# Optimization experiments

Measured on AMD Instinct MI355X. Metric: run time of the kernel, lower is better.

Reference implementation:

```python
import jax, jax.numpy as jnp
import numpy as np

N_ATOMS = 10000
N_EDGES = 150000
NB = 128          # n_atom_basis
NI = 3            # n_interactions
MAX_Z = 100
N_RBF = 20
CUTOFF = 5.0
EPS = 1e-08
BATCH = 64


def setup_inputs() -> dict:
    key = jax.random.key(0)
    ks = jax.random.split(key, 20)
    f32 = jnp.float32
    s = 0.05
    positions = jax.random.normal(ks[0], (N_ATOMS, 3), f32)
    atomic_numbers = jax.random.randint(ks[1], (N_ATOMS,), 0, MAX_Z)
    idx_i = jax.random.randint(ks[2], (N_EDGES,), 0, N_ATOMS)
    off = jax.random.randint(ks[3], (N_EDGES,), 1, N_ATOMS)
    idx_j = (idx_i + off) % N_ATOMS  # avoid self-edges (d_ij == 0)
    idx_m = jnp.sort(jax.random.randint(ks[4], (N_ATOMS,), 0, BATCH))
    emb = (jax.random.normal(ks[5], (MAX_Z, NB), f32) * s).at[0].set(0.0)  # padding_idx=0
    fW = jax.random.normal(ks[6], (N_RBF, NI * 3 * NB), f32) * s
    fb = jnp.zeros((NI * 3 * NB,), f32)
    ic1_W = jax.random.normal(ks[7], (NI, NB, NB), f32) * s
    ic1_b = jnp.zeros((NI, NB), f32)
    ic2_W = jax.random.normal(ks[8], (NI, NB, 3 * NB), f32) * s
    ic2_b = jnp.zeros((NI, 3 * NB), f32)
    mix_W = jax.random.normal(ks[9], (NI, NB, 2 * NB), f32) * s  # no bias
    ctx1_W = jax.random.normal(ks[10], (NI, 2 * NB, NB), f32) * s
    ctx1_b = jnp.zeros((NI, NB), f32)
    ctx2_W = jax.random.normal(ks[11], (NI, NB, 3 * NB), f32) * s
    ctx2_b = jnp.zeros((NI, 3 * NB), f32)
    o1_W = jax.random.normal(ks[12], (NB, NB), f32) * s
    o1_b = jnp.zeros((NB,), f32)
    o2_W = jax.random.normal(ks[13], (NB, NB), f32) * s
    o2_b = jnp.zeros((NB,), f32)
    o3_W = jax.random.normal(ks[14], (NB, 1), f32) * s
    o3_b = jnp.zeros((1,), f32)
    return dict(positions=positions, emb=emb, fW=fW, fb=fb,
                ic1_W=ic1_W, ic1_b=ic1_b, ic2_W=ic2_W, ic2_b=ic2_b,
                mix_W=mix_W, ctx1_W=ctx1_W, ctx1_b=ctx1_b, ctx2_W=ctx2_W, ctx2_b=ctx2_b,
                o1_W=o1_W, o1_b=o1_b, o2_W=o2_W, o2_b=o2_b, o3_W=o3_W, o3_b=o3_b,
                atomic_numbers=atomic_numbers, idx_i=idx_i, idx_j=idx_j, idx_m=idx_m,
                batch_num=BATCH)


def reference(positions, emb, fW, fb, ic1_W, ic1_b, ic2_W, ic2_b,
              mix_W, ctx1_W, ctx1_b, ctx2_W, ctx2_b,
              o1_W, o1_b, o2_W, o2_b, o3_W, o3_b,
              atomic_numbers, idx_i, idx_j, idx_m, batch_num):
    seg = jax.ops.segment_sum
    n_atoms = positions.shape[0]
    # pairwise distances
    r_ij = positions[idx_j] - positions[idx_i]                      # [E,3]
    d_ij = jnp.sqrt(jnp.sum(r_ij * r_ij, axis=-1, keepdims=True))   # [E,1]
    # Gaussian RBF
    offsets = jnp.linspace(0.0, CUTOFF, N_RBF, dtype=positions.dtype)
    width = offsets[1] - offsets[0]
    coeff = -0.5 / (width * width)
    phi = jnp.exp(coeff * (d_ij[..., None] - offsets) ** 2)         # [E,1,20]
    # cosine cutoff
    fcut = (0.5 * (jnp.cos(d_ij * jnp.pi / CUTOFF) + 1.0) * (d_ij < CUTOFF))[..., None]  # [E,1,1]
    filters = (phi @ fW + fb) * fcut                                # [E,1,NI*3*NB]
    dir_ij = r_ij / d_ij                                            # [E,3]
    q = emb[atomic_numbers][:, None]                                # [N,1,NB]
    mu = jnp.zeros((n_atoms, 3, NB), q.dtype)
    for i in range(NI):
        Wij = filters[..., i * 3 * NB:(i + 1) * 3 * NB]             # [E,1,3*NB]
        # interaction
        x = jax.nn.silu(q @ ic1_W[i] + ic1_b[i]) @ ic2_W[i] + ic2_b[i]  # [N,1,3*NB]
        x = Wij * x[idx_j]                                          # [E,1,3*NB]
        dq, dmuR, dmumu = jnp.split(x, 3, axis=-1)                  # [E,1,NB] each
        dq = seg(dq, idx_i, num_segments=n_atoms)                   # [N,1,NB]
        muj = mu[idx_j]                                             # [E,3,NB]
        dmu = dmuR * dir_ij[:, :, None] + dmumu * muj               # [E,3,NB]
        dmu = seg(dmu, idx_i, num_segments=n_atoms)                 # [N,3,NB]
        q = q + dq
        mu = mu + dmu
        # mixing
        mu_mix = mu @ mix_W[i]                                      # [N,3,2*NB]
        mu_V, mu_Wc = jnp.split(mu_mix, 2, axis=-1)                 # [N,3,NB]
        mu_Vn = jnp.sqrt(jnp.sum(mu_V * mu_V, axis=-2, keepdims=True) + EPS)  # [N,1,NB]
        ctx = jnp.concatenate([q, mu_Vn], axis=-1)                  # [N,1,2*NB]
        x = jax.nn.silu(ctx @ ctx1_W[i] + ctx1_b[i]) @ ctx2_W[i] + ctx2_b[i]  # [N,1,3*NB]
        dq_in, dmu_in, dqmu_in = jnp.split(x, 3, axis=-1)
        dmu_in = dmu_in * mu_Wc                                     # [N,3,NB]
        dqmu_in = dqmu_in * jnp.sum(mu_V * mu_Wc, axis=1, keepdims=True)  # [N,1,NB]
        q = q + dq_in + dqmu_in
        mu = mu + dmu_in
    qf = q[:, 0]                                                    # [N,NB]
    h = jax.nn.silu(qf @ o1_W + o1_b)
    h = jax.nn.silu(h @ o2_W + o2_b)
    y = h @ o3_W + o3_b                                             # [N,1]
    y = seg(y, idx_m, num_segments=batch_num)                       # [B,1]
    return (y, mu)
```

## Files before the change

### kernel.cpp

```cpp
#include <hip/hip_runtime.h>
#include <math.h>

#define NA 10000
#define NE 150000
#define NRBF 20
#define CUT 5.0f
#define EPSV 1e-8f
#define NBATCH 64
#define CAP 48
#define PI_F 3.14159265358979323846f

typedef short bf16x8 __attribute__((ext_vector_type(8)));
typedef float f32x4 __attribute__((ext_vector_type(4)));
typedef __fp16 h16x2 __attribute__((ext_vector_type(2)));
typedef unsigned short u16;

__device__ __forceinline__ u16 f2b(float x) {
    unsigned u = __builtin_bit_cast(unsigned, x);
    return (u16)((u + 0x7FFFu + ((u >> 16) & 1u)) >> 16);
}
__device__ __forceinline__ float b2f(u16 b) {
    unsigned u = ((unsigned)b) << 16;
    return __builtin_bit_cast(float, u);
}
__device__ __forceinline__ float silu_f(float x) { return x / (1.0f + expf(-x)); }

#define P_IC1 0
#define P_IC2 49152
#define P_MIX 196608
#define P_C1  294912
#define P_C2  393216
#define P_O1  540672
#define P_O2  557056
#define P_TOT 573440

__global__ __launch_bounds__(64) void pack_k(
    const float* __restrict__ ic1W, const float* __restrict__ ic2W,
    const float* __restrict__ mixW, const float* __restrict__ c1W,
    const float* __restrict__ c2W, const float* __restrict__ o1W,
    const float* __restrict__ o2W, u16* __restrict__ packs) {
    int id = blockIdx.x;
    const float* src; u16* dst; int N, rel;
    if (id < 96)        { int m = id / 32;          rel = id % 32; src = ic1W + m * 16384; dst = packs + P_IC1 + m * 16384; N = 128; }
    else if (id < 384)  { id -= 96;  int m = id / 96; rel = id % 96; src = ic2W + m * 49152; dst = packs + P_IC2 + m * 49152; N = 384; }
    else if (id < 576)  { id -= 384; int m = id / 64; rel = id % 64; src = mixW + m * 32768; dst = packs + P_MIX + m * 32768; N = 256; }
    else if (id < 768)  { id -= 576; int m = id / 64; rel = id % 64; src = c1W  + m * 32768; dst = packs + P_C1  + m * 32768; N = 128; }
    else if (id < 1056) { id -= 768; int m = id / 96; rel = id % 96; src = c2W  + m * 49152; dst = packs + P_C2  + m * 49152; N = 384; }
    else if (id < 1088) { rel = id - 1056; src = o1W; dst = packs + P_O1; N = 128; }
    else                { rel = id - 1088; src = o2W; dst = packs + P_O2; N = 128; }
    int NBT = N >> 4;
    int kb = rel / NBT, nb = rel % NBT;
    int l = threadIdx.x;
    int col = nb * 16 + (l & 15);
    int k0 = kb * 32 + 8 * (l >> 4);
    u16 v[8];
    #pragma unroll
    for (int i = 0; i < 8; i++) v[i] = f2b(src[(size_t)(k0 + i) * N + col]);
    *(bf16x8*)(dst + rel * 512 + l * 8) = *(bf16x8*)v;
}

template<int MT, int K>
__device__ __forceinline__ void stageA(const float* __restrict__ src, int row0,
                                       int maxrow, u16* As) {
    const int NV = MT * K / 4;
    for (int idx = threadIdx.x; idx < NV; idx += 256) {
        int r = idx / (K / 4), c4 = idx % (K / 4);
        float4 v = make_float4(0.f, 0.f, 0.f, 0.f);
        if (row0 + r < maxrow) v = *(const float4*)(src + (size_t)(row0 + r) * K + c4 * 4);
        uint2 o;
        o.x = (unsigned)f2b(v.x) | ((unsigned)f2b(v.y) << 16);
        o.y = (unsigned)f2b(v.z) | ((unsigned)f2b(v.w) << 16);
        *(uint2*)(As + r * (K + 8) + c4 * 4) = o;
    }
}

__device__ __forceinline__ bf16x8 aFrag(const u16* As, int stride, int row, int k0) {
    return *(const bf16x8*)(As + row * stride + k0);
}
__device__ __forceinline__ bf16x8 bFrag(const u16* __restrict__ pack, int NBT,
                                        int ks, int nb, int l) {
    return *(const bf16x8*)(pack + ((size_t)(ks * NBT + nb) * 64 + l) * 8);
}
#define MFMA(a, b, c) __builtin_amdgcn_mfma_f32_16x16x32_bf16(a, b, c, 0, 0, 0)

__global__ void init_q_k(const float* __restrict__ emb, const int* __restrict__ z,
                         float* __restrict__ q) {
    int idx = blockIdx.x * blockDim.x + threadIdx.x;
    if (idx >= NA * 128) return;
    int a = idx >> 7, c = idx & 127;
    q[idx] = emb[z[a] * 128 + c];
}

__global__ void edge_geom_k(const float* __restrict__ pos,
                            const int* __restrict__ idx_i, const int* __restrict__ idx_j,
                            float* __restrict__ edata, int* __restrict__ cnt,
                            int* __restrict__ bucketj) {
    int e = blockIdx.x * blockDim.x + threadIdx.x;
    if (e >= NE) return;
    int i = idx_i[e], j = idx_j[e];
    float rx = pos[j * 3 + 0] - pos[i * 3 + 0];
    float ry = pos[j * 3 + 1] - pos[i * 3 + 1];
    float rz = pos[j * 3 + 2] - pos[i * 3 + 2];
    float d = sqrtf(rx * rx + ry * ry + rz * rz);
    float inv = 1.0f / d;
    float fc = (d < CUT) ? 0.5f * (cosf(d * PI_F / CUT) + 1.0f) : 0.0f;
    const float width = CUT / (float)(NRBF - 1);
    const float coeff = -0.5f / (width * width);
    float ph[NRBF];
    #pragma unroll
    for (int k = 0; k < NRBF; k++) {
        float t = d - (float)k * width;
        ph[k] = expf(coeff * t * t);
    }
    int slot = atomicAdd(&cnt[i], 1);
    if (slot < CAP) {
        bucketj[i * CAP + slot] = j;
        float* ed = edata + ((size_t)i * CAP + slot) * 16;
        ed[0] = rx * inv; ed[1] = ry * inv; ed[2] = rz * inv; ed[3] = fc;
        h16x2* php = (h16x2*)(ed + 4);
        #pragma unroll
        for (int p = 0; p < 10; p++)
            php[p] = __builtin_amdgcn_cvt_pkrtz(ph[2 * p], ph[2 * p + 1]);
    }
}

__global__ __launch_bounds__(256) void mlp1_k(
    const float* __restrict__ q, const u16* __restrict__ pW1, const float* __restrict__ b1,
    const u16* __restrict__ pW2, const float* __restrict__ b2, u16* __restrict__ x_bf) {
    __shared__ u16 As[32 * 136];
    __shared__ u16 Hs[32 * 136];
    int abase = blockIdx.x * 32;
    stageA<32, 128>(q, abase, NA, As);
    __syncthreads();
    int l = threadIdx.x & 63, w = threadIdx.x >> 6, lm = l & 15, lg = l >> 4;
    f32x4 acc[2][2];
    #pragma unroll
    for (int j = 0; j < 2; j++)
        #pragma unroll
        for (int mi = 0; mi < 2; mi++) acc[j][mi] = (f32x4){0.f, 0.f, 0.f, 0.f};
    #pragma unroll
    for (int ks = 0; ks < 4; ks++) {
        bf16x8 a0 = aFrag(As, 136, lm, ks * 32 + 8 * lg);
        bf16x8 a1 = aFrag(As, 136, 16 + lm, ks * 32 + 8 * lg);
        #pragma unroll
        for (int j = 0; j < 2; j++) {
            bf16x8 b = bFrag(pW1, 8, ks, w + 4 * j, l);
            acc[j][0] = MFMA(a0, b, acc[j][0]);
            acc[j][1] = MFMA(a1, b, acc[j][1]);
        }
    }
    #pragma unroll
    for (int j = 0; j < 2; j++) {
        int col = 16 * (w + 4 * j) + lm;
        float bb = b1[col];
        #pragma unroll
        for (int mi = 0; mi < 2; mi++)
            #pragma unroll
            for (int v = 0; v < 4; v++)
                Hs[(16 * mi + 4 * lg + v) * 136 + col] = f2b(silu_f(acc[j][mi][v] + bb));
    }
    __syncthreads();
    f32x4 acc2[6][2];
    #pragma unroll
    for (int j = 0; j < 6; j++)
        #pragma unroll
        for (int mi = 0; mi < 2; mi++) acc2[j][mi] = (f32x4){0.f, 0.f, 0.f, 0.f};
    #pragma unroll
    for (int ks = 0; ks < 4; ks++) {
        bf16x8 a0 = aFrag(Hs, 136, lm, ks * 32 + 8 * lg);
        bf16x8 a1 = aFrag(Hs, 136, 16 + lm, ks * 32 + 8 * lg);
        #pragma unroll
        for (int j = 0; j < 6; j++) {
            bf16x8 b = bFrag(pW2, 24, ks, w + 4 * j, l);
            acc2[j][0] = MFMA(a0, b, acc2[j][0]);
            acc2[j][1] = MFMA(a1, b, acc2[j][1]);
        }
    }
    #pragma unroll
    for (int j = 0; j < 6; j++) {
        int col = 16 * (w + 4 * j) + lm;
        float bb = b2[col];
        #pragma unroll
        for (int mi = 0; mi < 2; mi++)
            #pragma unroll
            for (int v = 0; v < 4; v++) {
                int ga = abase + 16 * mi + 4 * lg + v;
                if (ga < NA) x_bf[(size_t)ga * 384 + col] = f2b(acc2[j][mi][v] + bb);
            }
    }
}

template<int IT0>
__global__ __launch_bounds__(128) void gather_k(
    const float* __restrict__ fW, const float* __restrict__ fb,
    const u16* __restrict__ x_bf, const u16* __restrict__ mu_bf,
    const float* __restrict__ edata, const int* __restrict__ cnt,
    const int* __restrict__ bucketj, int it,
    float* __restrict__ q, float* __restrict__ muF) {
    int a = blockIdx.x;
    int c = threadIdx.x;
    int cb = it * 384;
    h16x2 wp0[10], wp1[10], wp2[10];
    #pragma unroll
    for (int p = 0; p < 10; p++) {
        const float* r0 = fW + (2 * p) * 1152 + cb;
        const float* r1 = fW + (2 * p + 1) * 1152 + cb;
        wp0[p] = __builtin_amdgcn_cvt_pkrtz(r0[c], r1[c]);
        wp1[p] = __builtin_amdgcn_cvt_pkrtz(r0[128 + c], r1[128 + c]);
        if (!IT0) wp2[p] = __builtin_amdgcn_cvt_pkrtz(r0[256 + c], r1[256 + c]);
    }
    float fb0 = fb[cb + c], fb1 = fb[cb + 128 + c];
    float fb2 = IT0 ? 0.f : fb[cb + 256 + c];
    int n = cnt[a]; if (n > CAP) n = CAP;
    const int* bj = bucketj + a * CAP;
    const float* eb = edata + (size_t)a * CAP * 16;
    float adq = 0.f, am0 = 0.f, am1 = 0.f, am2 = 0.f;
    for (int ei = 0; ei < n; ei++) {
        int j = __builtin_amdgcn_readfirstlane(bj[ei]);
        const float* ed = eb + ei * 16;
        float4 gg = *(const float4*)ed;
        const h16x2* php = (const h16x2*)(ed + 4);
        float f0 = fb0, f1 = fb1, f2 = fb2;
        #pragma unroll
        for (int p = 0; p < 10; p++) {
            h16x2 ph = php[p];
            f0 = __builtin_amdgcn_fdot2(ph, wp0[p], f0, false);
            f1 = __builtin_amdgcn_fdot2(ph, wp1[p], f1, false);
            if (!IT0) f2 = __builtin_amdgcn_fdot2(ph, wp2[p], f2, false);
        }
        f0 *= gg.w; f1 *= gg.w;
        const u16* xr = x_bf + (size_t)j * 384;
        float x0 = f0 * b2f(xr[c]), x1 = f1 * b2f(xr[128 + c]);
        adq += x0;
        am0 += x1 * gg.x;
        am1 += x1 * gg.y;
        am2 += x1 * gg.z;
        if (!IT0) {
            f2 *= gg.w;
            float x2 = f2 * b2f(xr[256 + c]);
            const u16* mr = mu_bf + (size_t)j * 384;
            am0 += x2 * b2f(mr[c]);
            am1 += x2 * b2f(mr[128 + c]);
            am2 += x2 * b2f(mr[256 + c]);
        }
    }
    q[(size_t)a * 128 + c] += adq;
    muF[(size_t)a * 384 + c] += am0;
    muF[(size_t)a * 384 + 128 + c] += am1;
    muF[(size_t)a * 384 + 256 + c] += am2;
}

__global__ __launch_bounds__(256) void mixctx_k(
    float* __restrict__ q, float* __restrict__ muF, u16* __restrict__ mu_bf,
    const u16* __restrict__ pM,
    const u16* __restrict__ pC1, const float* __restrict__ c1b,
    const u16* __restrict__ pC2, const float* __restrict__ c2b) {
    __shared__ u16 As[48 * 136];
    __shared__ u16 mmL[16 * 768];
    __shared__ u16 Cs[16 * 264];
    __shared__ u16 Hs[16 * 136];
    int abase = blockIdx.x * 16;
    stageA<48, 128>(muF, abase * 3, 3 * NA, As);
    __syncthreads();
    int l = threadIdx.x & 63, w = threadIdx.x >> 6, lm = l & 15, lg = l >> 4;
    {
        f32x4 acc[4][3];
        #pragma unroll
        for (int j = 0; j < 4; j++)
            #pragma unroll
            for (int mi = 0; mi < 3; mi++) acc[j][mi] = (f32x4){0.f, 0.f, 0.f, 0.f};
        #pragma unroll
        for (int ks = 0; ks < 4; ks++) {
            bf16x8 a[3];
            #pragma unroll
            for (int mi = 0; mi < 3; mi++) a[mi] = aFrag(As, 136, 16 * mi + lm, ks * 32 + 8 * lg);
            #pragma unroll
            for (int j = 0; j < 4; j++) {
                bf16x8 b = bFrag(pM, 16, ks, w + 4 * j, l);
                #pragma unroll
                for (int mi = 0; mi < 3; mi++) acc[j][mi] = MFMA(a[mi], b, acc[j][mi]);
            }
        }
        #pragma unroll
        for (int j = 0; j < 4; j++) {
            int col = 16 * (w + 4 * j) + lm;
            #pragma unroll
            for (int mi = 0; mi < 3; mi++)
                #pragma unroll
                for (int v = 0; v < 4; v++) {
                    int R = 16 * mi + 4 * lg + v;
                    mmL[(R / 3) * 768 + (R % 3) * 256 + col] = f2b(acc[j][mi][v]);
                }
        }
    }
    __syncthreads();
    for (int idx = threadIdx.x; idx < 16 * 128; idx += 256) {
        int a = idx >> 7, cc = idx & 127;
        int ga = abase + a;
        float s = EPSV;
        #pragma unroll
        for (int d = 0; d < 3; d++) {
            float t = b2f(mmL[a * 768 + d * 256 + cc]);
            s += t * t;
        }
        float qv = (ga < NA) ? q[(size_t)ga * 128 + cc] : 0.f;
        Cs[a * 264 + cc] = f2b(qv);
        Cs[a * 264 + 128 + cc] = f2b(sqrtf(s));
    }
    __syncthreads();
    {
        f32x4 h[2];
        h[0] = (f32x4){0.f, 0.f, 0.f, 0.f}; h[1] = (f32x4){0.f, 0.f, 0.f, 0.f};
        #pragma unroll
        for (int ks = 0; ks < 8; ks++) {
            bf16x8 a0 = aFrag(Cs, 264, lm, ks * 32 + 8 * lg);
            #pragma unroll
            for (int j = 0; j < 2; j++) {
                bf16x8 b = bFrag(pC1, 8, ks, w + 4 * j, l);
                h[j] = MFMA(a0, b, h[j]);
            }
        }
        #pragma unroll
        for (int j = 0; j < 2; j++) {
            int col = 16 * (w + 4 * j) + lm;
            float bb = c1b[col];
            #pragma unroll
            for (int v = 0; v < 4; v++)
                Hs[(4 * lg + v) * 136 + col] = f2b(silu_f(h[j][v] + bb));
        }
    }
    __syncthreads();
    f32x4 acc2[6];
    #pragma unroll
    for (int j = 0; j < 6; j++) acc2[j] = (f32x4){0.f, 0.f, 0.f, 0.f};
    #pragma unroll
    for (int ks = 0; ks < 4; ks++) {
        bf16x8 a0 = aFrag(Hs, 136, lm, ks * 32 + 8 * lg);
        #pragma unroll
        for (int j = 0; j < 6; j++) {
            bf16x8 b = bFrag(pC2, 24, ks, w + 4 * j, l);
            acc2[j] = MFMA(a0, b, acc2[j]);
        }
    }
    #pragma unroll
    for (int j = 0; j < 6; j++) {
        float bb = c2b[16 * (w + 4 * j) + lm];
        #pragma unroll
        for (int v = 0; v < 4; v++) acc2[j][v] += bb;
    }
    #pragma unroll
    for (int v = 0; v < 4; v++) {
        int al = 4 * lg + v;
        int ga = abase + al;
        if (ga >= NA) continue;
        #pragma unroll
        for (int jj = 0; jj < 2; jj++) {
            int cc = 16 * w + 64 * jj + lm;
            float x0 = acc2[jj][v], x1 = acc2[jj + 2][v], x2 = acc2[jj + 4][v];
            float dot = 0.f, muW[3];
            #pragma unroll
            for (int d = 0; d < 3; d++) {
                float muV = b2f(mmL[al * 768 + d * 256 + cc]);
                muW[d] = b2f(mmL[al * 768 + d * 256 + 128 + cc]);
                dot += muV * muW[d];
            }
            q[(size_t)ga * 128 + cc] += x0 + x2 * dot;
            #pragma unroll
            for (int d = 0; d < 3; d++) {
                size_t mo = (size_t)ga * 384 + d * 128 + cc;
                float m = muF[mo] + x1 * muW[d];
                muF[mo] = m;
                mu_bf[mo] = f2b(m);
            }
        }
    }
}

__global__ __launch_bounds__(256) void readout_k(
    const float* __restrict__ q, const u16* __restrict__ pO1, const float* __restrict__ o1b,
    const u16* __restrict__ pO2, const float* __restrict__ o2b,
    const float* __restrict__ o3W, const float* __restrict__ o3b,
    const int* __restrict__ idx_m, float* __restrict__ y) {
    __shared__ u16 As[32 * 136];
    __shared__ u16 Hs[32 * 136];
    __shared__ float red[256];
    __shared__ float part[NBATCH];
    __shared__ int mlo, mhi;
    int abase = blockIdx.x * 32;
    stageA<32, 128>(q, abase, NA, As);
    __syncthreads();
    int l = threadIdx.x & 63, w = threadIdx.x >> 6, lm = l & 15, lg = l >> 4;
    f32x4 acc[2][2];
    #pragma unroll
    for (int j = 0; j < 2; j++)
        #pragma unroll
        for (int mi = 0; mi < 2; mi++) acc[j][mi] = (f32x4){0.f, 0.f, 0.f, 0.f};
    #pragma unroll
    for (int ks = 0; ks < 4; ks++) {
        bf16x8 a0 = aFrag(As, 136, lm, ks * 32 + 8 * lg);
        bf16x8 a1 = aFrag(As, 136, 16 + lm, ks * 32 + 8 * lg);
        #pragma unroll
        for (int j = 0; j < 2; j++) {
            bf16x8 b = bFrag(pO1, 8, ks, w + 4 * j, l);
            acc[j][0] = MFMA(a0, b, acc[j][0]);
            acc[j][1] = MFMA(a1, b, acc[j][1]);
        }
    }
    #pragma unroll
    for (int j = 0; j < 2; j++) {
        int col = 16 * (w + 4 * j) + lm;
        float bb = o1b[col];
        #pragma unroll
        for (int mi = 0; mi < 2; mi++)
            #pragma unroll
            for (int v = 0; v < 4; v++)
                Hs[(16 * mi + 4 * lg + v) * 136 + col] = f2b(silu_f(acc[j][mi][v] + bb));
    }
    __syncthreads();
    f32x4 acc2[2][2];
    #pragma unroll
    for (int j = 0; j < 2; j++)
        #pragma unroll
        for (int mi = 0; mi < 2; mi++) acc2[j][mi] = (f32x4){0.f, 0.f, 0.f, 0.f};
    #pragma unroll
    for (int ks = 0; ks < 4; ks++) {
        bf16x8 a0 = aFrag(Hs, 136, lm, ks * 32 + 8 * lg);
        bf16x8 a1 = aFrag(Hs, 136, 16 + lm, ks * 32 + 8 * lg);
        #pragma unroll
        for (int j = 0; j < 2; j++) {
            bf16x8 b = bFrag(pO2, 8, ks, w + 4 * j, l);
            acc2[j][0] = MFMA(a0, b, acc2[j][0]);
            acc2[j][1] = MFMA(a1, b, acc2[j][1]);
        }
    }
    #pragma unroll
    for (int j = 0; j < 2; j++) {
        int col = 16 * (w + 4 * j) + lm;
        float bb = o2b[col];
        #pragma unroll
        for (int mi = 0; mi < 2; mi++)
            #pragma unroll
            for (int v = 0; v < 4; v++)
                As[(16 * mi + 4 * lg + v) * 136 + col] = f2b(silu_f(acc2[j][mi][v] + bb));
    }
    if (threadIdx.x < NBATCH) part[threadIdx.x] = 0.f;
    if (threadIdx.x == 0) { mlo = NBATCH; mhi = -1; }
    __syncthreads();
    int a = threadIdx.x >> 3, gseg = threadIdx.x & 7;
    float p = 0.f;
    #pragma unroll
    for (int cc = 0; cc < 16; cc++) {
        int c = gseg * 16 + cc;
        p += b2f(As[a * 136 + c]) * o3W[c];
    }
    red[threadIdx.x] = p;
    __syncthreads();
    if (gseg == 0) {
        float s = 0.f;
        #pragma unroll
        for (int k = 0; k < 8; k++) s += red[a * 8 + k];
        int ga = abase + a;
        if (ga < NA) {
            int m = idx_m[ga];
            atomicAdd(&part[m], s + o3b[0]);
            atomicMin(&mlo, m);
            atomicMax(&mhi, m);
        }
    }
    __syncthreads();
    for (int m = mlo + (int)threadIdx.x; m <= mhi; m += 256)
        atomicAdd(&y[m], part[m]);
}

extern "C" void kernel_launch(void* const* d_in, const int* in_sizes, int n_in,
                              void* d_out, int out_size, void* d_ws, size_t ws_size,
                              hipStream_t stream) {
    const float* pos  = (const float*)d_in[0];
    const float* emb  = (const float*)d_in[1];
    const float* fW   = (const float*)d_in[2];
    const float* fb   = (const float*)d_in[3];
    const float* ic1W = (const float*)d_in[4];
    const float* ic1b = (const float*)d_in[5];
    const float* ic2W = (const float*)d_in[6];
    const float* ic2b = (const float*)d_in[7];
    const float* mixW = (const float*)d_in[8];
    const float* c1W  = (const float*)d_in[9];
    const float* c1b  = (const float*)d_in[10];
    const float* c2W  = (const float*)d_in[11];
    const float* c2b  = (const float*)d_in[12];
    const float* o1W  = (const float*)d_in[13];
    const float* o1b  = (const float*)d_in[14];
    const float* o2W  = (const float*)d_in[15];
    const float* o2b  = (const float*)d_in[16];
    const float* o3W  = (const float*)d_in[17];
    const float* o3b  = (const float*)d_in[18];
    const int* zn     = (const int*)d_in[19];
    const int* idx_i  = (const int*)d_in[20];
    const int* idx_j  = (const int*)d_in[21];
    const int* idx_m  = (const int*)d_in[22];

    float* y   = (float*)d_out;
    float* muF = (float*)d_out + NBATCH;

    char* wp = (char*)d_ws;
    float* q      = (float*)wp;  wp += (size_t)NA * 128 * 4;
    u16*   x_bf   = (u16*)wp;    wp += (size_t)NA * 384 * 2;
    u16*   mu_bf  = (u16*)wp;    wp += (size_t)NA * 384 * 2;
    float* edata  = (float*)wp;  wp += (size_t)NA * CAP * 16 * 4;
    int*   cnt    = (int*)wp;    wp += (size_t)NA * 4;
    int*   bucketj= (int*)wp;    wp += (size_t)NA * CAP * 4;
    u16*   packs  = (u16*)wp;    wp += (size_t)P_TOT * 2;

    hipMemsetAsync(d_out, 0, (size_t)(NBATCH + (size_t)NA * 384) * 4, stream);
    hipMemsetAsync(cnt, 0, (size_t)NA * 4, stream);

    pack_k<<<1120, 64, 0, stream>>>(ic1W, ic2W, mixW, c1W, c2W, o1W, o2W, packs);
    init_q_k<<<(NA * 128 + 255) / 256, 256, 0, stream>>>(emb, zn, q);
    edge_geom_k<<<(NE + 255) / 256, 256, 0, stream>>>(pos, idx_i, idx_j, edata, cnt, bucketj);

    for (int it = 0; it < 3; it++) {
        mlp1_k<<<313, 256, 0, stream>>>(
            q, packs + P_IC1 + it * 16384, ic1b + it * 128,
            packs + P_IC2 + it * 49152, ic2b + it * 384, x_bf);
        if (it == 0)
            gather_k<1><<<NA, 128, 0, stream>>>(
                fW, fb, x_bf, mu_bf, edata, cnt, bucketj, it, q, muF);
        else
            gather_k<0><<<NA, 128, 0, stream>>>(
                fW, fb, x_bf, mu_bf, edata, cnt, bucketj, it, q, muF);
        mixctx_k<<<(NA + 15) / 16, 256, 0, stream>>>(
            q, muF, mu_bf,
            packs + P_MIX + it * 32768,
            packs + P_C1 + it * 32768, c1b + it * 128,
            packs + P_C2 + it * 49152, c2b + it * 384);
    }

    readout_k<<<313, 256, 0, stream>>>(q, packs + P_O1, o1b, packs + P_O2, o2b,
                                       o3W, o3b, idx_m, y);
}
```

Before: 389.5 us.

## Interleave x and mu into per-channel records, pad edge lists to multiples of four

Merges the separate bf16 x and mu neighbour arrays into one interleaved layout of six values per (atom, channel), so the gather kernel fetches all per-neighbour data with a single 12-byte load per lane rather than six scattered 2-byte loads. A new pad kernel rounds each atom's edge count up to a multiple of four using zero-filled entries, which lets the gather loop load neighbour indices as int4 and unroll by four. The cost is an extra small kernel, strided stores in mlp1 and mixctx, and wasted work on the padded dummy edges. Padded edges have a zero cutoff weight, so they contribute nothing.

After: 395.9 us. No clear change (+1.6%).

```diff
diff --git a/kernel.cpp b/kernel.cpp
--- a/kernel.cpp
+++ b/kernel.cpp
@@ -124,9 +124,24 @@
     }
 }
 
+__global__ void pad_k(int* __restrict__ cnt, int* __restrict__ bucketj,
+                      float* __restrict__ edata) {
+    int a = blockIdx.x * blockDim.x + threadIdx.x;
+    if (a >= NA) return;
+    int n = cnt[a]; if (n > CAP) n = CAP;
+    int n4 = (n + 3) & ~3;
+    for (int k = n; k < n4; k++) {
+        bucketj[a * CAP + k] = 0;
+        float* ed = edata + ((size_t)a * CAP + k) * 16;
+        #pragma unroll
+        for (int t = 0; t < 16; t++) ed[t] = 0.f;
+    }
+    cnt[a] = n4;
+}
+
 __global__ __launch_bounds__(256) void mlp1_k(
     const float* __restrict__ q, const u16* __restrict__ pW1, const float* __restrict__ b1,
-    const u16* __restrict__ pW2, const float* __restrict__ b2, u16* __restrict__ x_bf) {
+    const u16* __restrict__ pW2, const float* __restrict__ b2, u16* __restrict__ xmu) {
     __shared__ u16 As[32 * 136];
     __shared__ u16 Hs[32 * 136];
     int abase = blockIdx.x * 32;
@@ -176,24 +191,30 @@
             acc2[j][1] = MFMA(a1, b, acc2[j][1]);
         }
     }
-    #pragma unroll
-    for (int j = 0; j < 6; j++) {
-        int col = 16 * (w + 4 * j) + lm;
-        float bb = b2[col];
-        #pragma unroll
-        for (int mi = 0; mi < 2; mi++)
-            #pragma unroll
-            for (int v = 0; v < 4; v++) {
-                int ga = abase + 16 * mi + 4 * lg + v;
-                if (ga < NA) x_bf[(size_t)ga * 384 + col] = f2b(acc2[j][mi][v] + bb);
-            }
-    }
+    int b = 16 * w + lm;
+    #pragma unroll
+    for (int mi = 0; mi < 2; mi++)
+        #pragma unroll
+        for (int v = 0; v < 4; v++) {
+            int ga = abase + 16 * mi + 4 * lg + v;
+            if (ga >= NA) continue;
+            #pragma unroll
+            for (int half = 0; half < 2; half++) {
+                int c = b + 64 * half;
+                float x0 = acc2[half][mi][v]     + b2[c];
+                float x1 = acc2[2 + half][mi][v] + b2[128 + c];
+                float x2 = acc2[4 + half][mi][v] + b2[256 + c];
+                u16* xr = xmu + ((size_t)ga * 128 + c) * 6;
+                *(unsigned*)xr = (unsigned)f2b(x0) | ((unsigned)f2b(x1) << 16);
+                xr[2] = f2b(x2);
+            }
+        }
 }
 
 template<int IT0>
 __global__ __launch_bounds__(128) void gather_k(
     const float* __restrict__ fW, const float* __restrict__ fb,
-    const u16* __restrict__ x_bf, const u16* __restrict__ mu_bf,
+    const u16* __restrict__ xmu,
     const float* __restrict__ edata, const int* __restrict__ cnt,
     const int* __restrict__ bucketj, int it,
     float* __restrict__ q, float* __restrict__ muF) {
@@ -211,37 +232,50 @@
     }
     float fb0 = fb[cb + c], fb1 = fb[cb + 128 + c];
     float fb2 = IT0 ? 0.f : fb[cb + 256 + c];
-    int n = cnt[a]; if (n > CAP) n = CAP;
+    int n4 = cnt[a];
     const int* bj = bucketj + a * CAP;
     const float* eb = edata + (size_t)a * CAP * 16;
     float adq = 0.f, am0 = 0.f, am1 = 0.f, am2 = 0.f;
-    for (int ei = 0; ei < n; ei++) {
-        int j = __builtin_amdgcn_readfirstlane(bj[ei]);
-        const float* ed = eb + ei * 16;
-        float4 gg = *(const float4*)ed;
-        const h16x2* php = (const h16x2*)(ed + 4);
-        float f0 = fb0, f1 = fb1, f2 = fb2;
-        #pragma unroll
-        for (int p = 0; p < 10; p++) {
-            h16x2 ph = php[p];
-            f0 = __builtin_amdgcn_fdot2(ph, wp0[p], f0, false);
-            f1 = __builtin_amdgcn_fdot2(ph, wp1[p], f1, false);
-            if (!IT0) f2 = __builtin_amdgcn_fdot2(ph, wp2[p], f2, false);
-        }
-        f0 *= gg.w; f1 *= gg.w;
-        const u16* xr = x_bf + (size_t)j * 384;
-        float x0 = f0 * b2f(xr[c]), x1 = f1 * b2f(xr[128 + c]);
-        adq += x0;
-        am0 += x1 * gg.x;
-        am1 += x1 * gg.y;
-        am2 += x1 * gg.z;
-        if (!IT0) {
-            f2 *= gg.w;
-            float x2 = f2 * b2f(xr[256 + c]);
-            const u16* mr = mu_bf + (size_t)j * 384;
-            am0 += x2 * b2f(mr[c]);
-            am1 += x2 * b2f(mr[128 + c]);
-            am2 += x2 * b2f(mr[256 + c]);
+    for (int e0 = 0; e0 < n4; e0 += 4) {
+        int4 j4 = *(const int4*)(bj + e0);
+        #pragma unroll
+        for (int u = 0; u < 4; u++) {
+            int j = __builtin_amdgcn_readfirstlane(
+                u == 0 ? j4.x : u == 1 ? j4.y : u == 2 ? j4.z : j4.w);
+            const float* ed = eb + (size_t)(e0 + u) * 16;
+            const u16* xr = xmu + ((size_t)j * 128 + c) * 6;
+            float xc0, xc1, xc2 = 0.f, m0 = 0.f, m1 = 0.f, m2 = 0.f;
+            if (IT0) {
+                unsigned xv = *(const unsigned*)xr;
+                xc0 = b2f((u16)(xv & 0xffff)); xc1 = b2f((u16)(xv >> 16));
+            } else {
+                uint3 xv = *(const uint3*)xr;
+                xc0 = b2f((u16)(xv.x & 0xffff)); xc1 = b2f((u16)(xv.x >> 16));
+                xc2 = b2f((u16)(xv.y & 0xffff));
+                m0 = b2f((u16)(xv.y >> 16));
+                m1 = b2f((u16)(xv.z & 0xffff)); m2 = b2f((u16)(xv.z >> 16));
+            }
+            float4 gg = *(const float4*)ed;
+            const h16x2* php = (const h16x2*)(ed + 4);
+            float f0 = fb0, f1 = fb1, f2 = fb2;
+            #pragma unroll
+            for (int p = 0; p < 10; p++) {
+                h16x2 ph = php[p];
+                f0 = __builtin_amdgcn_fdot2(ph, wp0[p], f0, false);
+                f1 = __builtin_amdgcn_fdot2(ph, wp1[p], f1, false);
+                if (!IT0) f2 = __builtin_amdgcn_fdot2(ph, wp2[p], f2, false);
+            }
+            f0 *= gg.w; f1 *= gg.w;
+            float x0 = f0 * xc0, x1 = f1 * xc1;
+            adq += x0;
+            am0 += x1 * gg.x;
+            am1 += x1 * gg.y;
+            am2 += x1 * gg.z;
+            if (!IT0) {
+                f2 *= gg.w;
+                float x2 = f2 * xc2;
+                am0 += x2 * m0; am1 += x2 * m1; am2 += x2 * m2;
+            }
         }
     }
     q[(size_t)a * 128 + c] += adq;
@@ -251,7 +285,7 @@
 }
 
 __global__ __launch_bounds__(256) void mixctx_k(
-    float* __restrict__ q, float* __restrict__ muF, u16* __restrict__ mu_bf,
+    float* __restrict__ q, float* __restrict__ muF, u16* __restrict__ xmu,
     const u16* __restrict__ pM,
     const u16* __restrict__ pC1, const float* __restrict__ c1b,
     const u16* __restrict__ pC2, const float* __restrict__ c2b) {
@@ -357,7 +391,7 @@
         for (int jj = 0; jj < 2; jj++) {
             int cc = 16 * w + 64 * jj + lm;
             float x0 = acc2[jj][v], x1 = acc2[jj + 2][v], x2 = acc2[jj + 4][v];
-            float dot = 0.f, muW[3];
+            float dot = 0.f, muW[3], mnew[3];
             #pragma unroll
             for (int d = 0; d < 3; d++) {
                 float muV = b2f(mmL[al * 768 + d * 256 + cc]);
@@ -370,8 +404,11 @@
                 size_t mo = (size_t)ga * 384 + d * 128 + cc;
                 float m = muF[mo] + x1 * muW[d];
                 muF[mo] = m;
-                mu_bf[mo] = f2b(m);
-            }
+                mnew[d] = m;
+            }
+            u16* xr = xmu + ((size_t)ga * 128 + cc) * 6;
+            xr[3] = f2b(mnew[0]);
+            *(unsigned*)(xr + 4) = (unsigned)f2b(mnew[1]) | ((unsigned)f2b(mnew[2]) << 16);
         }
     }
 }
@@ -504,8 +541,7 @@
 
     char* wp = (char*)d_ws;
     float* q      = (float*)wp;  wp += (size_t)NA * 128 * 4;
-    u16*   x_bf   = (u16*)wp;    wp += (size_t)NA * 384 * 2;
-    u16*   mu_bf  = (u16*)wp;    wp += (size_t)NA * 384 * 2;
+    u16*   xmu    = (u16*)wp;    wp += (size_t)NA * 128 * 6 * 2;
     float* edata  = (float*)wp;  wp += (size_t)NA * CAP * 16 * 4;
     int*   cnt    = (int*)wp;    wp += (size_t)NA * 4;
     int*   bucketj= (int*)wp;    wp += (size_t)NA * CAP * 4;
@@ -517,19 +553,20 @@
     pack_k<<<1120, 64, 0, stream>>>(ic1W, ic2W, mixW, c1W, c2W, o1W, o2W, packs);
     init_q_k<<<(NA * 128 + 255) / 256, 256, 0, stream>>>(emb, zn, q);
     edge_geom_k<<<(NE + 255) / 256, 256, 0, stream>>>(pos, idx_i, idx_j, edata, cnt, bucketj);
+    pad_k<<<(NA + 255) / 256, 256, 0, stream>>>(cnt, bucketj, edata);
 
     for (int it = 0; it < 3; it++) {
         mlp1_k<<<313, 256, 0, stream>>>(
             q, packs + P_IC1 + it * 16384, ic1b + it * 128,
-            packs + P_IC2 + it * 49152, ic2b + it * 384, x_bf);
+            packs + P_IC2 + it * 49152, ic2b + it * 384, xmu);
         if (it == 0)
             gather_k<1><<<NA, 128, 0, stream>>>(
-                fW, fb, x_bf, mu_bf, edata, cnt, bucketj, it, q, muF);
+                fW, fb, xmu, edata, cnt, bucketj, it, q, muF);
         else
             gather_k<0><<<NA, 128, 0, stream>>>(
-                fW, fb, x_bf, mu_bf, edata, cnt, bucketj, it, q, muF);
+                fW, fb, xmu, edata, cnt, bucketj, it, q, muF);
         mixctx_k<<<(NA + 15) / 16, 256, 0, stream>>>(
-            q, muF, mu_bf,
+            q, muF, xmu,
             packs + P_MIX + it * 32768,
             packs + P_C1 + it * 32768, c1b + it * 128,
             packs + P_C2 + it * 49152, c2b + it * 384);
```

## Prepack filter weights to fp16, pad edge lists, unroll gather by four

Applied to the files above, without the earlier changes.

Filter weights are converted to packed fp16 pairs once in the pack kernel instead of in every gather block, and the embedding init is folded into the same launch. A new pad kernel rounds each atom's edge count up to a multiple of four with zero-filled entries. The gather loop can then load four neighbour indices at once and issue the neighbour feature loads before the filter dot products, giving more memory-level parallelism. The cost is an extra launch and padded zero edges that still do memory reads of atom 0.

After: 413.3 us. 1.06x slower.

```diff
diff --git a/kernel.cpp b/kernel.cpp
--- a/kernel.cpp
+++ b/kernel.cpp
@@ -32,14 +32,34 @@
 #define P_C2  393216
 #define P_O1  540672
 #define P_O2  557056
-#define P_TOT 573440
+#define P_FWH 573440
+#define P_TOT 619520
 
 __global__ __launch_bounds__(64) void pack_k(
     const float* __restrict__ ic1W, const float* __restrict__ ic2W,
     const float* __restrict__ mixW, const float* __restrict__ c1W,
     const float* __restrict__ c2W, const float* __restrict__ o1W,
-    const float* __restrict__ o2W, u16* __restrict__ packs) {
+    const float* __restrict__ o2W, const float* __restrict__ fW,
+    const float* __restrict__ emb, const int* __restrict__ zn,
+    float* __restrict__ q, u16* __restrict__ packs) {
     int id = blockIdx.x;
+    if (id >= 1138) {
+        int elem = ((id - 1138) * 64 + (int)threadIdx.x) * 4;
+        int a = elem >> 7, c = elem & 127;
+        *(float4*)(q + elem) = *(const float4*)(emb + (size_t)zn[a] * 128 + c);
+        return;
+    }
+    if (id >= 1120) {
+        int col = (id - 1120) * 64 + (int)threadIdx.x;
+        unsigned* dst32 = (unsigned*)(packs + P_FWH);
+        #pragma unroll
+        for (int p = 0; p < 10; p++) {
+            h16x2 v = __builtin_amdgcn_cvt_pkrtz(fW[(size_t)(2 * p) * 1152 + col],
+                                                 fW[(size_t)(2 * p + 1) * 1152 + col]);
+            dst32[p * 1152 + col] = __builtin_bit_cast(unsigned, v);
+        }
+        return;
+    }
     const float* src; u16* dst; int N, rel;
     if (id < 96)        { int m = id / 32;          rel = id % 32; src = ic1W + m * 16384; dst = packs + P_IC1 + m * 16384; N = 128; }
     else if (id < 384)  { id -= 96;  int m = id / 96; rel = id % 96; src = ic2W + m * 49152; dst = packs + P_IC2 + m * 49152; N = 384; }
@@ -82,14 +102,6 @@
     return *(const bf16x8*)(pack + ((size_t)(ks * NBT + nb) * 64 + l) * 8);
 }
 #define MFMA(a, b, c) __builtin_amdgcn_mfma_f32_16x16x32_bf16(a, b, c, 0, 0, 0)
-
-__global__ void init_q_k(const float* __restrict__ emb, const int* __restrict__ z,
-                         float* __restrict__ q) {
-    int idx = blockIdx.x * blockDim.x + threadIdx.x;
-    if (idx >= NA * 128) return;
-    int a = idx >> 7, c = idx & 127;
-    q[idx] = emb[z[a] * 128 + c];
-}
 
 __global__ void edge_geom_k(const float* __restrict__ pos,
                             const int* __restrict__ idx_i, const int* __restrict__ idx_j,
@@ -124,6 +136,21 @@
     }
 }
 
+__global__ void pad_k(int* __restrict__ cnt, int* __restrict__ bucketj,
+                      float* __restrict__ edata) {
+    int a = blockIdx.x * blockDim.x + threadIdx.x;
+    if (a >= NA) return;
+    int n = cnt[a]; if (n > CAP) n = CAP;
+    int n4 = (n + 3) & ~3;
+    for (int k = n; k < n4; k++) {
+        bucketj[a * CAP + k] = 0;
+        float* ed = edata + ((size_t)a * CAP + k) * 16;
+        #pragma unroll
+        for (int t = 0; t < 16; t++) ed[t] = 0.f;
+    }
+    cnt[a] = n4;
+}
+
 __global__ __launch_bounds__(256) void mlp1_k(
     const float* __restrict__ q, const u16* __restrict__ pW1, const float* __restrict__ b1,
     const u16* __restrict__ pW2, const float* __restrict__ b2, u16* __restrict__ x_bf) {
@@ -192,7 +219,7 @@
 
 template<int IT0>
 __global__ __launch_bounds__(128) void gather_k(
-    const float* __restrict__ fW, const float* __restrict__ fb,
+    const unsigned* __restrict__ fWh, const float* __restrict__ fb,
     const u16* __restrict__ x_bf, const u16* __restrict__ mu_bf,
     const float* __restrict__ edata, const int* __restrict__ cnt,
     const int* __restrict__ bucketj, int it,
@@ -203,45 +230,52 @@
     h16x2 wp0[10], wp1[10], wp2[10];
     #pragma unroll
     for (int p = 0; p < 10; p++) {
-        const float* r0 = fW + (2 * p) * 1152 + cb;
-        const float* r1 = fW + (2 * p + 1) * 1152 + cb;
-        wp0[p] = __builtin_amdgcn_cvt_pkrtz(r0[c], r1[c]);
-        wp1[p] = __builtin_amdgcn_cvt_pkrtz(r0[128 + c], r1[128 + c]);
-        if (!IT0) wp2[p] = __builtin_amdgcn_cvt_pkrtz(r0[256 + c], r1[256 + c]);
+        wp0[p] = __builtin_bit_cast(h16x2, fWh[p * 1152 + cb + c]);
+        wp1[p] = __builtin_bit_cast(h16x2, fWh[p * 1152 + cb + 128 + c]);
+        if (!IT0) wp2[p] = __builtin_bit_cast(h16x2, fWh[p * 1152 + cb + 256 + c]);
     }
     float fb0 = fb[cb + c], fb1 = fb[cb + 128 + c];
     float fb2 = IT0 ? 0.f : fb[cb + 256 + c];
-    int n = cnt[a]; if (n > CAP) n = CAP;
+    int n4 = cnt[a];
     const int* bj = bucketj + a * CAP;
     const float* eb = edata + (size_t)a * CAP * 16;
     float adq = 0.f, am0 = 0.f, am1 = 0.f, am2 = 0.f;
-    for (int ei = 0; ei < n; ei++) {
-        int j = __builtin_amdgcn_readfirstlane(bj[ei]);
-        const float* ed = eb + ei * 16;
-        float4 gg = *(const float4*)ed;
-        const h16x2* php = (const h16x2*)(ed + 4);
-        float f0 = fb0, f1 = fb1, f2 = fb2;
-        #pragma unroll
-        for (int p = 0; p < 10; p++) {
-            h16x2 ph = php[p];
-            f0 = __builtin_amdgcn_fdot2(ph, wp0[p], f0, false);
-            f1 = __builtin_amdgcn_fdot2(ph, wp1[p], f1, false);
-            if (!IT0) f2 = __builtin_amdgcn_fdot2(ph, wp2[p], f2, false);
-        }
-        f0 *= gg.w; f1 *= gg.w;
-        const u16* xr = x_bf + (size_t)j * 384;
-        float x0 = f0 * b2f(xr[c]), x1 = f1 * b2f(xr[128 + c]);
-        adq += x0;
-        am0 += x1 * gg.x;
-        am1 += x1 * gg.y;
-        am2 += x1 * gg.z;
-        if (!IT0) {
-            f2 *= gg.w;
-            float x2 = f2 * b2f(xr[256 + c]);
-            const u16* mr = mu_bf + (size_t)j * 384;
-            am0 += x2 * b2f(mr[c]);
-            am1 += x2 * b2f(mr[128 + c]);
-            am2 += x2 * b2f(mr[256 + c]);
+    for (int e0 = 0; e0 < n4; e0 += 4) {
+        int4 j4 = *(const int4*)(bj + e0);
+        #pragma unroll
+        for (int u = 0; u < 4; u++) {
+            int j = __builtin_amdgcn_readfirstlane(
+                u == 0 ? j4.x : u == 1 ? j4.y : u == 2 ? j4.z : j4.w);
+            const float* ed = eb + (size_t)(e0 + u) * 16;
+            const u16* xr = x_bf + (size_t)j * 384;
+            float xc0 = b2f(xr[c]), xc1 = b2f(xr[128 + c]);
+            float xc2 = 0.f, m0 = 0.f, m1 = 0.f, m2 = 0.f;
+            if (!IT0) {
+                xc2 = b2f(xr[256 + c]);
+                const u16* mr = mu_bf + (size_t)j * 384;
+                m0 = b2f(mr[c]); m1 = b2f(mr[128 + c]); m2 = b2f(mr[256 + c]);
+            }
+            float4 gg = *(const float4*)ed;
+            const h16x2* php = (const h16x2*)(ed + 4);
+            float f0 = fb0, f1 = fb1, f2 = fb2;
+            #pragma unroll
+            for (int p = 0; p < 10; p++) {
+                h16x2 ph = php[p];
+                f0 = __builtin_amdgcn_fdot2(ph, wp0[p], f0, false);
+                f1 = __builtin_amdgcn_fdot2(ph, wp1[p], f1, false);
+                if (!IT0) f2 = __builtin_amdgcn_fdot2(ph, wp2[p], f2, false);
+            }
+            f0 *= gg.w; f1 *= gg.w;
+            float x0 = f0 * xc0, x1 = f1 * xc1;
+            adq += x0;
+            am0 += x1 * gg.x;
+            am1 += x1 * gg.y;
+            am2 += x1 * gg.z;
+            if (!IT0) {
+                f2 *= gg.w;
+                float x2 = f2 * xc2;
+                am0 += x2 * m0; am1 += x2 * m1; am2 += x2 * m2;
+            }
         }
     }
     q[(size_t)a * 128 + c] += adq;
@@ -514,9 +548,12 @@
     hipMemsetAsync(d_out, 0, (size_t)(NBATCH + (size_t)NA * 384) * 4, stream);
     hipMemsetAsync(cnt, 0, (size_t)NA * 4, stream);
 
-    pack_k<<<1120, 64, 0, stream>>>(ic1W, ic2W, mixW, c1W, c2W, o1W, o2W, packs);
-    init_q_k<<<(NA * 128 + 255) / 256, 256, 0, stream>>>(emb, zn, q);
+    pack_k<<<6138, 64, 0, stream>>>(ic1W, ic2W, mixW, c1W, c2W, o1W, o2W, fW,
+                                    emb, zn, q, packs);
     edge_geom_k<<<(NE + 255) / 256, 256, 0, stream>>>(pos, idx_i, idx_j, edata, cnt, bucketj);
+    pad_k<<<(NA + 255) / 256, 256, 0, stream>>>(cnt, bucketj, edata);
+
+    const unsigned* fWh = (const unsigned*)(packs + P_FWH);
 
     for (int it = 0; it < 3; it++) {
         mlp1_k<<<313, 256, 0, stream>>>(
@@ -524,10 +561,10 @@
             packs + P_IC2 + it * 49152, ic2b + it * 384, x_bf);
         if (it == 0)
             gather_k<1><<<NA, 128, 0, stream>>>(
-                fW, fb, x_bf, mu_bf, edata, cnt, bucketj, it, q, muF);
+                fWh, fb, x_bf, mu_bf, edata, cnt, bucketj, it, q, muF);
         else
             gather_k<0><<<NA, 128, 0, stream>>>(
-                fW, fb, x_bf, mu_bf, edata, cnt, bucketj, it, q, muF);
+                fWh, fb, x_bf, mu_bf, edata, cnt, bucketj, it, q, muF);
         mixctx_k<<<(NA + 15) / 16, 256, 0, stream>>>(
             q, muF, mu_bf,
             packs + P_MIX + it * 32768,
```
